# Kernel optimization log

Measured on AMD Instinct MI355X. Metric: run time of the kernel, lower is better.

Reference implementation:

```python
import jax, jax.numpy as jnp
import numpy as np

N, E, F_IN, HID, L, G = 50000, 800000, 128, 64, 3, 512
BN_EPS = 1e-5


def setup_inputs() -> dict:
    key = jax.random.key(0)
    ks = jax.random.split(key, 8)
    x = jax.random.normal(ks[0], (N, F_IN), dtype=jnp.float32)
    edge_index = jax.random.randint(ks[1], (2, E), 0, N, dtype=jnp.int32)
    batch = jnp.sort(jax.random.randint(ks[2], (N,), 0, G, dtype=jnp.int32))
    # params (Glorot-ish init for weights; BN init per module: gamma=1, beta=1e-4)
    W_feat = jax.random.normal(ks[3], (F_IN, HID), dtype=jnp.float32) / np.sqrt(F_IN)
    b_feat = jnp.zeros((HID,), jnp.float32)
    Ws = jax.random.normal(ks[4], (L, HID, HID), dtype=jnp.float32) / np.sqrt(HID)
    bs = jnp.zeros((L, HID), jnp.float32)
    bn_feat_g = jnp.ones((F_IN,), jnp.float32)
    bn_feat_b = jnp.full((F_IN,), 1e-4, jnp.float32)
    bn_g = jnp.ones((L, HID), jnp.float32)
    bn_b = jnp.full((L, HID), 1e-4, jnp.float32)
    return {"x": x, "edge_index": edge_index, "batch": batch,
            "bn_feat_g": bn_feat_g, "bn_feat_b": bn_feat_b,
            "W_feat": W_feat, "b_feat": b_feat,
            "bn_g": bn_g, "bn_b": bn_b, "Ws": Ws, "bs": bs}


def batch_norm(x, gamma, beta):
    # training-mode BatchNorm1d: biased variance over the node dimension
    mu = jnp.mean(x, axis=0)
    var = jnp.mean(jnp.square(x - mu), axis=0)
    return (x - mu) * jax.lax.rsqrt(var + BN_EPS) * gamma + beta


def gcn_conv(h, W, b, src, dst):
    # h: [N, d_in] -> linear then normalized gather-scatter with self-loops
    h = h @ W  # [N, d_out]
    n = h.shape[0]
    loop = jnp.arange(n, dtype=src.dtype)
    row = jnp.concatenate([src, loop])  # source (j)
    col = jnp.concatenate([dst, loop])  # target (i)
    w = jnp.ones(row.shape[0], h.dtype)
    deg = jax.ops.segment_sum(w, row, num_segments=n)  # PyG: deg over row
    dis = jnp.where(deg > 0, jax.lax.rsqrt(jnp.maximum(deg, 1.0)), 0.0)
    norm = dis[row] * w * dis[col]  # [E+N]
    out = jax.ops.segment_sum(norm[:, None] * h[row], col, num_segments=n)
    return out + b


def reference(x, edge_index, batch, bn_feat_g, bn_feat_b, W_feat, b_feat,
              bn_g, bn_b, Ws, bs):
    src, dst = edge_index[0], edge_index[1]
    h = batch_norm(x, bn_feat_g, bn_feat_b)
    h = jax.nn.relu(h @ W_feat + b_feat)  # conv_feat has gfn=True -> plain linear
    for i in range(L):
        h = batch_norm(h, bn_g[i], bn_b[i])
        h = jax.nn.relu(gcn_conv(h, Ws[i], bs[i], src, dst))
    graph_emb = jax.ops.segment_sum(h, batch, num_segments=G)  # global_add_pool
    return graph_emb
```

## Files before the change

### kernel.cpp

```cpp
#include <hip/hip_runtime.h>
#include <math.h>

#define HID 64
#define BN_EPS 1e-5f
#define NBMAX 256

typedef unsigned int uint;
typedef unsigned short ushort;


__global__ __launch_bounds__(256) void k_bucket_hist(const int* __restrict__ ei, int E, int NB,
                                                     int* __restrict__ bcnt_d, int* __restrict__ bcnt_s) {
    __shared__ int hd[NBMAX], hs[NBMAX];
    int t = threadIdx.x;
    if (t < NB) { hd[t] = 0; hs[t] = 0; }
    __syncthreads();
    for (int e = blockIdx.x * 256 + t; e < E; e += gridDim.x * 256) {
        int src = ei[e], dst = ei[E + e];
        atomicAdd(&hs[src >> 8], 1);
        atomicAdd(&hd[dst >> 8], 1);
    }
    __syncthreads();
    if (t < NB) {
        if (hd[t]) atomicAdd(&bcnt_d[t], hd[t]);
        if (hs[t]) atomicAdd(&bcnt_s[t], hs[t]);
    }
}

__global__ __launch_bounds__(256) void k_bucket_scan(const int* __restrict__ bcnt_d, const int* __restrict__ bcnt_s,
                                                     int NB, int N, int E,
                                                     int* __restrict__ bbase_d, int* __restrict__ cursor_d,
                                                     int* __restrict__ bbase_s, int* __restrict__ cursor_s,
                                                     int* __restrict__ rowptr) {
    __shared__ int sh[256];
    int t = threadIdx.x;
    int v = (t < NB) ? bcnt_d[t] : 0;
    sh[t] = v; __syncthreads();
    for (int s = 1; s < 256; s <<= 1) { int u = (t >= s) ? sh[t - s] : 0; __syncthreads(); sh[t] += u; __syncthreads(); }
    int excl = sh[t] - v;
    if (t <= NB) bbase_d[t] = excl;
    if (t < NB) cursor_d[t] = excl;
    if (t == 0) rowptr[N] = E;
    __syncthreads();
    v = (t < NB) ? bcnt_s[t] : 0;
    sh[t] = v; __syncthreads();
    for (int s = 1; s < 256; s <<= 1) { int u = (t >= s) ? sh[t - s] : 0; __syncthreads(); sh[t] += u; __syncthreads(); }
    excl = sh[t] - v;
    if (t <= NB) bbase_s[t] = excl;
    if (t < NB) cursor_s[t] = excl;
}

__global__ __launch_bounds__(256) void k_scatter_stats(const int* __restrict__ ei, int E, int NB, int SCB,
                                                       int* __restrict__ cursor_d, int* __restrict__ cursor_s,
                                                       uint* __restrict__ bedge, int* __restrict__ bsrc,
                                                       const float* __restrict__ X, int n,
                                                       float* __restrict__ spartial) {
    __shared__ __align__(16) char smemraw[8192];
    int t = threadIdx.x;
    if ((int)blockIdx.x < SCB) {
        int* hd = (int*)smemraw;
        int* hs = hd + 256;
        int* curd = hs + 256;
        int* curs = curd + 256;
        int chunk = (E + SCB - 1) / SCB;
        int e0 = blockIdx.x * chunk;
        int e1 = min(e0 + chunk, E);
        if (t < NB) { hd[t] = 0; hs[t] = 0; }
        __syncthreads();
        for (int e = e0 + t; e < e1; e += 256) {
            int src = ei[e], dst = ei[E + e];
            atomicAdd(&hd[dst >> 8], 1);
            atomicAdd(&hs[src >> 8], 1);
        }
        __syncthreads();
        if (t < NB) {
            curd[t] = hd[t] ? atomicAdd(&cursor_d[t], hd[t]) : 0;
            curs[t] = hs[t] ? atomicAdd(&cursor_s[t], hs[t]) : 0;
        }
        __syncthreads();
        for (int e = e0 + t; e < e1; e += 256) {
            int src = ei[e], dst = ei[E + e];
            int pd = atomicAdd(&curd[dst >> 8], 1);
            bedge[pd] = ((uint)(dst & 255) << 16) | (uint)src;
            int ps = atomicAdd(&curs[src >> 8], 1);
            bsrc[ps] = src;
        }
    } else {
        int b = blockIdx.x - SCB;
        int SB = gridDim.x - SCB;
        float4* shs = (float4*)smemraw;
        float4* shq = shs + 256;
        int c4 = t & 31, rsub = t >> 5;
        float4 s = make_float4(0.f, 0.f, 0.f, 0.f);
        float4 q = make_float4(0.f, 0.f, 0.f, 0.f);
        for (int r = b * 8 + rsub; r < n; r += SB * 8) {
            float4 v = ((const float4*)X)[(size_t)r * 32 + c4];
            s.x += v.x; s.y += v.y; s.z += v.z; s.w += v.w;
            q.x = fmaf(v.x, v.x, q.x); q.y = fmaf(v.y, v.y, q.y);
            q.z = fmaf(v.z, v.z, q.z); q.w = fmaf(v.w, v.w, q.w);
        }
        shs[t] = s; shq[t] = q;
        __syncthreads();
        if (rsub == 0) {
            #pragma unroll
            for (int k = 1; k < 8; k++) {
                float4 a = shs[t + k * 32], bq = shq[t + k * 32];
                s.x += a.x; s.y += a.y; s.z += a.z; s.w += a.w;
                q.x += bq.x; q.y += bq.y; q.z += bq.z; q.w += bq.w;
            }
            float* p = spartial + (size_t)b * 256;
            ((float4*)p)[c4] = s;
            ((float4*)(p + 128))[c4] = q;
        }
    }
}

__global__ __launch_bounds__(256) void k_build_csr_outdeg_statsf(
        const uint* __restrict__ bedge, const int* __restrict__ bbase_d,
        const int* __restrict__ bsrc, const int* __restrict__ bbase_s,
        int N, int NB,
        int* __restrict__ rowptr, int* __restrict__ eidx, float* __restrict__ dis,
        const float* __restrict__ spartial, int snblocks, float* __restrict__ stats) {
    __shared__ int h[256], off[256], cur[256];
    int t = threadIdx.x, b = blockIdx.x;
    if (b < NB) {
        int base = bbase_d[b], end = bbase_d[b + 1];
        h[t] = 0; __syncthreads();
        for (int p = base + t; p < end; p += 256)
            atomicAdd(&h[(int)(bedge[p] >> 16) & 255], 1);
        __syncthreads();
        off[t] = h[t]; __syncthreads();
        for (int s = 1; s < 256; s <<= 1) { int u = (t >= s) ? off[t - s] : 0; __syncthreads(); off[t] += u; __syncthreads(); }
        int excl = off[t] - h[t];
        int node = (b << 8) + t;
        if (node <= N) rowptr[node] = base + excl;
        cur[t] = excl; __syncthreads();
        for (int p = base + t; p < end; p += 256) {
            uint be = bedge[p];
            int bin = (int)(be >> 16) & 255;
            int pos = atomicAdd(&cur[bin], 1);
            eidx[base + pos] = (int)(be & 0xffffu);
        }
    } else if (b < 2 * NB) {
        int b2 = b - NB;
        int base = bbase_s[b2], end = bbase_s[b2 + 1];
        h[t] = 0; __syncthreads();
        for (int p = base + t; p < end; p += 256) atomicAdd(&h[bsrc[p] & 255], 1);
        __syncthreads();
        int node = (b2 << 8) + t;
        if (node < N) dis[node] = rsqrtf((float)(h[t] + 1));
    } else {
        int j = b - 2 * NB;
        float* sh = (float*)h;
        float acc = 0.f;
        for (int bb = t; bb < snblocks; bb += 256) acc += spartial[(size_t)bb * 256 + j];
        sh[t] = acc;
        __syncthreads();
        #pragma unroll
        for (int o = 128; o > 0; o >>= 1) {
            if (t < o) sh[t] += sh[t + o];
            __syncthreads();
        }
        if (t == 0) stats[j] = sh[0];
    }
}

template <int F>
__global__ __launch_bounds__(256) void k_stats_final(const float* __restrict__ partial, int nblocks,
                                                     float* __restrict__ stats) {
    int j = blockIdx.x;
    int t = threadIdx.x;
    float acc = 0.f;
    for (int b = t; b < nblocks; b += 256) acc += partial[(size_t)b * (2 * F) + j];
    __shared__ float sh[256];
    sh[t] = acc;
    __syncthreads();
    #pragma unroll
    for (int off = 128; off > 0; off >>= 1) {
        if (t < off) sh[t] += sh[t + off];
        __syncthreads();
    }
    if (t == 0) stats[j] = sh[0];
}


__device__ inline uint bf16pk(float a, float b) {
    uint ua = __builtin_bit_cast(uint, a);
    ua += 0x7fff + ((ua >> 16) & 1);
    uint ub = __builtin_bit_cast(uint, b);
    ub += 0x7fff + ((ub >> 16) & 1);
    return (ua >> 16) | (ub & 0xffff0000u);
}
__device__ inline float bfl(uint v) { return __builtin_bit_cast(float, v << 16); }
__device__ inline float bfh(uint v) { return __builtin_bit_cast(float, v & 0xffff0000u); }

template <int K, bool RELU, bool DIS, bool STATS, bool HASB>
__global__ __launch_bounds__(256) void k_gemm(const float* __restrict__ X, const float* __restrict__ W,
                                              const float* __restrict__ stats,
                                              const float* __restrict__ gamma, const float* __restrict__ beta,
                                              const float* __restrict__ bias0, const float* __restrict__ dis,
                                              float n_inv, void* __restrict__ out, int n,
                                              float* __restrict__ spartial) {
    constexpr int KC = 64;
    constexpr int XS = 68;
    __shared__ float Xs[KC * XS];
    __shared__ float Wsm[KC * HID];
    __shared__ float As[128], Cs[128];

    int t = threadIdx.x;
    int tx = t & 15, ty = t >> 4;
    int row0 = blockIdx.x * 64;

    if (t < K) {
        float mu = stats[t] * n_inv;
        float var = stats[K + t] * n_inv - mu * mu;
        float a = gamma[t] * rsqrtf(var + BN_EPS);
        As[t] = a;
        Cs[t] = beta[t] - mu * a;
    }
    __syncthreads();

    float acc[4][4];
    #pragma unroll
    for (int i = 0; i < 4; i++)
        #pragma unroll
        for (int j = 0; j < 4; j++) acc[i][j] = 0.f;
    float4 bp = make_float4(0.f, 0.f, 0.f, 0.f);

    for (int kc = 0; kc < K; kc += KC) {
        #pragma unroll
        for (int it = 0; it < 4; ++it) {
            int id = t + 256 * it;
            int r = id >> 4, c4 = id & 15;
            float4 v = make_float4(0.f, 0.f, 0.f, 0.f);
            if (row0 + r < n) v = *(const float4*)(X + (size_t)(row0 + r) * K + kc + 4 * c4);
            int kk = 4 * c4;
            Xs[(kk + 0) * XS + r] = v.x;
            Xs[(kk + 1) * XS + r] = v.y;
            Xs[(kk + 2) * XS + r] = v.z;
            Xs[(kk + 3) * XS + r] = v.w;
        }
        {
            const float4* wsrc = (const float4*)(W + (size_t)kc * HID);
            #pragma unroll
            for (int it = 0; it < 4; ++it) {
                int id = t + 256 * it;
                int kl = id >> 4;
                float4 raw = wsrc[id];
                float a = As[kc + kl], c = Cs[kc + kl];
                float4 sc;
                sc.x = a * raw.x; sc.y = a * raw.y; sc.z = a * raw.z; sc.w = a * raw.w;
                ((float4*)Wsm)[id] = sc;
                bp.x = fmaf(c, raw.x, bp.x);
                bp.y = fmaf(c, raw.y, bp.y);
                bp.z = fmaf(c, raw.z, bp.z);
                bp.w = fmaf(c, raw.w, bp.w);
            }
        }
        __syncthreads();
        #pragma unroll 8
        for (int k = 0; k < KC; ++k) {
            float4 xv = *(const float4*)&Xs[k * XS + 4 * ty];
            float4 wv = *(const float4*)&Wsm[k * HID + 4 * tx];
            acc[0][0] = fmaf(xv.x, wv.x, acc[0][0]);
            acc[0][1] = fmaf(xv.x, wv.y, acc[0][1]);
            acc[0][2] = fmaf(xv.x, wv.z, acc[0][2]);
            acc[0][3] = fmaf(xv.x, wv.w, acc[0][3]);
            acc[1][0] = fmaf(xv.y, wv.x, acc[1][0]);
            acc[1][1] = fmaf(xv.y, wv.y, acc[1][1]);
            acc[1][2] = fmaf(xv.y, wv.z, acc[1][2]);
            acc[1][3] = fmaf(xv.y, wv.w, acc[1][3]);
            acc[2][0] = fmaf(xv.z, wv.x, acc[2][0]);
            acc[2][1] = fmaf(xv.z, wv.y, acc[2][1]);
            acc[2][2] = fmaf(xv.z, wv.z, acc[2][2]);
            acc[2][3] = fmaf(xv.z, wv.w, acc[2][3]);
            acc[3][0] = fmaf(xv.w, wv.x, acc[3][0]);
            acc[3][1] = fmaf(xv.w, wv.y, acc[3][1]);
            acc[3][2] = fmaf(xv.w, wv.z, acc[3][2]);
            acc[3][3] = fmaf(xv.w, wv.w, acc[3][3]);
        }
        __syncthreads();
    }

    {
        float* redb = Xs + 2048;
        *(float4*)&redb[ty * 64 + 4 * tx] = bp;
        __syncthreads();
        if (t < 64) {
            float s = 0.f;
            #pragma unroll
            for (int k = 0; k < 16; ++k) s += redb[k * 64 + t];
            Xs[3072 + t] = s + (HASB ? bias0[t] : 0.f);
        }
        __syncthreads();
    }
    float4 bv = *(const float4*)&Xs[3072 + 4 * tx];

    float4 cs = make_float4(0.f, 0.f, 0.f, 0.f);
    float4 cq = make_float4(0.f, 0.f, 0.f, 0.f);
    #pragma unroll
    for (int i = 0; i < 4; ++i) {
        int row = row0 + 4 * ty + i;
        bool valid = row < n;
        float vx = acc[i][0] + bv.x, vy = acc[i][1] + bv.y;
        float vz = acc[i][2] + bv.z, vw = acc[i][3] + bv.w;
        if constexpr (DIS) {
            if (valid) {
                float d = dis[row];
                uint2 pk;
                pk.x = bf16pk(vx * d, vy * d);
                pk.y = bf16pk(vz * d, vw * d);
                *(uint2*)((ushort*)out + (size_t)row * HID + 4 * tx) = pk;
            }
        } else {
            float4 v;
            v.x = RELU ? fmaxf(vx, 0.f) : vx;
            v.y = RELU ? fmaxf(vy, 0.f) : vy;
            v.z = RELU ? fmaxf(vz, 0.f) : vz;
            v.w = RELU ? fmaxf(vw, 0.f) : vw;
            if (valid) {
                *(float4*)((float*)out + (size_t)row * HID + 4 * tx) = v;
                if constexpr (STATS) {
                    cs.x += v.x; cs.y += v.y; cs.z += v.z; cs.w += v.w;
                    cq.x = fmaf(v.x, v.x, cq.x); cq.y = fmaf(v.y, v.y, cq.y);
                    cq.z = fmaf(v.z, v.z, cq.z); cq.w = fmaf(v.w, v.w, cq.w);
                }
            }
        }
    }
    if constexpr (STATS) {
        __syncthreads();
        float* reds = Xs;
        float* redq = Xs + 1024;
        *(float4*)&reds[ty * 64 + 4 * tx] = cs;
        *(float4*)&redq[ty * 64 + 4 * tx] = cq;
        __syncthreads();
        if (t < 64) {
            float s = 0.f, q = 0.f;
            #pragma unroll
            for (int k = 0; k < 16; ++k) { s += reds[k * 64 + t]; q += redq[k * 64 + t]; }
            spartial[(size_t)blockIdx.x * 128 + t] = s;
            spartial[(size_t)blockIdx.x * 128 + 64 + t] = q;
        }
    }
}


template <bool STATS>
__global__ __launch_bounds__(256) void k_agg(const ushort* __restrict__ s, const int* __restrict__ rowptr,
                                             const int* __restrict__ eidx, const float* __restrict__ dis,
                                             const float* __restrict__ bias, float* __restrict__ out, int n,
                                             float* __restrict__ spartial) {
    int t = threadIdx.x;
    int nl = t >> 5;
    int li = t & 31;
    int i = blockIdx.x * 8 + nl;
    int f = li * 2;
    float2 r = make_float2(0.f, 0.f);
    bool valid = i < n;
    if (valid) {
        const uint* sp = (const uint*)s;
        uint v = sp[(size_t)i * 32 + li];
        float ax = bfl(v), ay = bfh(v);
        int q = rowptr[i], qe = rowptr[i + 1];
        for (; q + 8 <= qe; q += 8) {
            int j0 = eidx[q], j1 = eidx[q + 1], j2 = eidx[q + 2], j3 = eidx[q + 3];
            int j4 = eidx[q + 4], j5 = eidx[q + 5], j6 = eidx[q + 6], j7 = eidx[q + 7];
            uint v0 = sp[(size_t)j0 * 32 + li];
            uint v1 = sp[(size_t)j1 * 32 + li];
            uint v2 = sp[(size_t)j2 * 32 + li];
            uint v3 = sp[(size_t)j3 * 32 + li];
            uint v4 = sp[(size_t)j4 * 32 + li];
            uint v5 = sp[(size_t)j5 * 32 + li];
            uint v6 = sp[(size_t)j6 * 32 + li];
            uint v7 = sp[(size_t)j7 * 32 + li];
            ax += ((bfl(v0) + bfl(v1)) + (bfl(v2) + bfl(v3))) + ((bfl(v4) + bfl(v5)) + (bfl(v6) + bfl(v7)));
            ay += ((bfh(v0) + bfh(v1)) + (bfh(v2) + bfh(v3))) + ((bfh(v4) + bfh(v5)) + (bfh(v6) + bfh(v7)));
        }
        for (; q + 4 <= qe; q += 4) {
            int j0 = eidx[q], j1 = eidx[q + 1], j2 = eidx[q + 2], j3 = eidx[q + 3];
            uint v0 = sp[(size_t)j0 * 32 + li];
            uint v1 = sp[(size_t)j1 * 32 + li];
            uint v2 = sp[(size_t)j2 * 32 + li];
            uint v3 = sp[(size_t)j3 * 32 + li];
            ax += (bfl(v0) + bfl(v1)) + (bfl(v2) + bfl(v3));
            ay += (bfh(v0) + bfh(v1)) + (bfh(v2) + bfh(v3));
        }
        for (; q < qe; ++q) {
            uint vv = sp[(size_t)eidx[q] * 32 + li];
            ax += bfl(vv); ay += bfh(vv);
        }
        float dd = dis[i];
        float2 bb = *(const float2*)(bias + f);
        r.x = fmaxf(fmaf(dd, ax, bb.x), 0.f);
        r.y = fmaxf(fmaf(dd, ay, bb.y), 0.f);
        *(float2*)(out + (size_t)i * HID + f) = r;
    }
    if constexpr (STATS) {
        __shared__ float sh[8 * 64 * 2];
        sh[nl * 64 + f] = r.x;
        sh[nl * 64 + f + 1] = r.y;
        sh[512 + nl * 64 + f] = r.x * r.x;
        sh[512 + nl * 64 + f + 1] = r.y * r.y;
        __syncthreads();
        if (t < 64) {
            float ss = 0.f, qq = 0.f;
            #pragma unroll
            for (int k = 0; k < 8; ++k) { ss += sh[k * 64 + t]; qq += sh[512 + k * 64 + t]; }
            spartial[(size_t)blockIdx.x * 128 + t] = ss;
            spartial[(size_t)blockIdx.x * 128 + 64 + t] = qq;
        }
    }
}


__global__ __launch_bounds__(256) void k_pool(const float* __restrict__ h, const int* __restrict__ batch,
                                              int n, float* __restrict__ out) {
    int g = blockIdx.x;
    int lo = 0, hi = n;
    while (lo < hi) { int mid = (lo + hi) >> 1; if (batch[mid] < g) lo = mid + 1; else hi = mid; }
    int start = lo;
    hi = n;
    while (lo < hi) { int mid = (lo + hi) >> 1; if (batch[mid] < g + 1) lo = mid + 1; else hi = mid; }
    int end = lo;
    int lane = threadIdx.x & 63;
    int rs = threadIdx.x >> 6;
    float acc = 0.f;
    for (int r = start + rs; r < end; r += 4) acc += h[(size_t)r * HID + lane];
    __shared__ float sh[256];
    sh[threadIdx.x] = acc;
    __syncthreads();
    if (threadIdx.x < 64) {
        acc = sh[threadIdx.x] + sh[64 + threadIdx.x] + sh[128 + threadIdx.x] + sh[192 + threadIdx.x];
        out[(size_t)g * HID + threadIdx.x] = acc;
    }
}


extern "C" void kernel_launch(void* const* d_in, const int* in_sizes, int n_in,
                              void* d_out, int out_size, void* d_ws, size_t ws_size,
                              hipStream_t stream) {
    const float* x     = (const float*)d_in[0];
    const int*   ei    = (const int*)d_in[1];
    const int*   batch = (const int*)d_in[2];
    const float* bnfg  = (const float*)d_in[3];
    const float* bnfb  = (const float*)d_in[4];
    const float* Wfeat = (const float*)d_in[5];
    const float* bfeat = (const float*)d_in[6];
    const float* bng   = (const float*)d_in[7];
    const float* bnb   = (const float*)d_in[8];
    const float* Ws    = (const float*)d_in[9];
    const float* bs    = (const float*)d_in[10];
    float* out = (float*)d_out;

    const int N   = in_sizes[2];
    const int E   = in_sizes[1] / 2;
    const int L   = in_sizes[9] / (HID * HID);
    const int G   = out_size / HID;
    const int NB  = (N + 255) >> 8;
    const int SCB = 256;
    const int SB  = 512;
    const int gG  = (N + 63) / 64;
    const int gA  = (N + 7) / 8;
    const float n_inv = 1.f / (float)N;

    char* w = (char*)d_ws;
    auto alloc = [&](size_t bytes) { char* p = w; w += (bytes + 255) & ~(size_t)255; return p; };
    int*   bcnt_d = (int*)alloc(256 * 4);
    int*   bcnt_s = (int*)alloc(256 * 4);
    size_t zero_bytes = (size_t)(w - (char*)d_ws);
    float* stats    = (float*)alloc(1024 * 4);
    size_t spmax    = (size_t)(SB > gA ? SB : gA) * 256 * 4;
    float* spartial = (float*)alloc(spmax);
    int*   bbase_d  = (int*)alloc(257 * 4);
    int*   cursor_d = (int*)alloc(256 * 4);
    int*   bbase_s  = (int*)alloc(257 * 4);
    int*   cursor_s = (int*)alloc(256 * 4);
    int*   rowptr   = (int*)alloc(((size_t)N + 1) * 4);
    int*   eidx     = (int*)alloc((size_t)E * 4);
    float* dis      = (float*)alloc((size_t)N * 4);
    float* bufA     = (float*)alloc((size_t)N * HID * 4);
    ushort* bufB    = (ushort*)alloc((size_t)N * HID * 2);
    uint* bedge = (uint*)bufA;
    int*  bsrc  = (int*)bufB;

    hipMemsetAsync(d_ws, 0, zero_bytes, stream);

    k_bucket_hist<<<512, 256, 0, stream>>>(ei, E, NB, bcnt_d, bcnt_s);
    k_bucket_scan<<<1, 256, 0, stream>>>(bcnt_d, bcnt_s, NB, N, E,
                                         bbase_d, cursor_d, bbase_s, cursor_s, rowptr);
    k_scatter_stats<<<SCB + SB, 256, 0, stream>>>(ei, E, NB, SCB, cursor_d, cursor_s,
                                                  bedge, bsrc, x, N, spartial);
    k_build_csr_outdeg_statsf<<<2 * NB + 256, 256, 0, stream>>>(
        bedge, bbase_d, bsrc, bbase_s, N, NB, rowptr, eidx, dis, spartial, SB, stats);

    k_gemm<128, true, false, true, true><<<gG, 256, 0, stream>>>(
        x, Wfeat, stats, bnfg, bnfb, bfeat, nullptr, n_inv, (void*)bufA, N, spartial);
    int spblocks = gG;

    for (int l = 0; l < L; ++l) {
        k_stats_final<64><<<128, 256, 0, stream>>>(spartial, spblocks, stats);
        k_gemm<64, false, true, false, false><<<gG, 256, 0, stream>>>(
            bufA, Ws + (size_t)l * HID * HID, stats, bng + (size_t)l * HID, bnb + (size_t)l * HID,
            nullptr, dis, n_inv, (void*)bufB, N, nullptr);
        if (l < L - 1) {
            k_agg<true><<<gA, 256, 0, stream>>>(bufB, rowptr, eidx, dis, bs + (size_t)l * HID, bufA, N, spartial);
            spblocks = gA;
        } else {
            k_agg<false><<<gA, 256, 0, stream>>>(bufB, rowptr, eidx, dis, bs + (size_t)l * HID, bufA, N, nullptr);
        }
    }

    k_pool<<<G, 256, 0, stream>>>(bufA, batch, N, out);
}
```

Measured before the change: 298.7 us.

## Fuse stats reductions via atomics, merge hist+scan, fuse pooling into last aggregation

Merges the bucket histogram and scan into one kernel using a last-block-done counter. Replaces per-block partial buffers plus separate final-reduction kernels with float atomicAdds straight into the stats arrays, which removes the k_stats_final launches. The final aggregation now accumulates global_add_pool directly through atomics over runs of sorted batch ids, so the k_pool kernel and the last feature write go away. The aggregation kernel is also restructured so each node is handled by 4 edge slots × 8 lanes using uint4 loads, with shuffle reductions. The trade-offs are atomic contention and nondeterministic float summation order.

```diff
diff --git a/kernel.cpp b/kernel.cpp
--- a/kernel.cpp
+++ b/kernel.cpp
@@ -9,11 +9,27 @@
 typedef unsigned short ushort;
 
 
-__global__ __launch_bounds__(256) void k_bucket_hist(const int* __restrict__ ei, int E, int NB,
-                                                     int* __restrict__ bcnt_d, int* __restrict__ bcnt_s) {
-    __shared__ int hd[NBMAX], hs[NBMAX];
+__device__ inline uint bf16pk(float a, float b) {
+    uint ua = __builtin_bit_cast(uint, a);
+    ua += 0x7fff + ((ua >> 16) & 1);
+    uint ub = __builtin_bit_cast(uint, b);
+    ub += 0x7fff + ((ub >> 16) & 1);
+    return (ua >> 16) | (ub & 0xffff0000u);
+}
+__device__ inline float bfl(uint v) { return __builtin_bit_cast(float, v << 16); }
+__device__ inline float bfh(uint v) { return __builtin_bit_cast(float, v & 0xffff0000u); }
+
+
+__global__ __launch_bounds__(256) void k_hist_scan(const int* __restrict__ ei, int E, int NB, int N,
+                                                   int* __restrict__ bcnt_d, int* __restrict__ bcnt_s,
+                                                   int* __restrict__ done,
+                                                   int* __restrict__ bbase_d, int* __restrict__ cursor_d,
+                                                   int* __restrict__ bbase_s, int* __restrict__ cursor_s,
+                                                   int* __restrict__ rowptr) {
+    __shared__ int hd[256], hs[256];
+    __shared__ int lastFlag;
     int t = threadIdx.x;
-    if (t < NB) { hd[t] = 0; hs[t] = 0; }
+    hd[t] = 0; hs[t] = 0;
     __syncthreads();
     for (int e = blockIdx.x * 256 + t; e < E; e += gridDim.x * 256) {
         int src = ei[e], dst = ei[E + e];
@@ -25,27 +41,23 @@
         if (hd[t]) atomicAdd(&bcnt_d[t], hd[t]);
         if (hs[t]) atomicAdd(&bcnt_s[t], hs[t]);
     }
-}
-
-__global__ __launch_bounds__(256) void k_bucket_scan(const int* __restrict__ bcnt_d, const int* __restrict__ bcnt_s,
-                                                     int NB, int N, int E,
-                                                     int* __restrict__ bbase_d, int* __restrict__ cursor_d,
-                                                     int* __restrict__ bbase_s, int* __restrict__ cursor_s,
-                                                     int* __restrict__ rowptr) {
-    __shared__ int sh[256];
-    int t = threadIdx.x;
-    int v = (t < NB) ? bcnt_d[t] : 0;
-    sh[t] = v; __syncthreads();
-    for (int s = 1; s < 256; s <<= 1) { int u = (t >= s) ? sh[t - s] : 0; __syncthreads(); sh[t] += u; __syncthreads(); }
-    int excl = sh[t] - v;
+    __threadfence();
+    __syncthreads();
+    if (t == 0) lastFlag = (atomicAdd(done, 1) == (int)gridDim.x - 1);
+    __syncthreads();
+    if (!lastFlag) return;
+    int v = (t < NB) ? atomicAdd(&bcnt_d[t], 0) : 0;
+    hd[t] = v; __syncthreads();
+    for (int s = 1; s < 256; s <<= 1) { int u = (t >= s) ? hd[t - s] : 0; __syncthreads(); hd[t] += u; __syncthreads(); }
+    int excl = hd[t] - v;
     if (t <= NB) bbase_d[t] = excl;
     if (t < NB) cursor_d[t] = excl;
     if (t == 0) rowptr[N] = E;
     __syncthreads();
-    v = (t < NB) ? bcnt_s[t] : 0;
-    sh[t] = v; __syncthreads();
-    for (int s = 1; s < 256; s <<= 1) { int u = (t >= s) ? sh[t - s] : 0; __syncthreads(); sh[t] += u; __syncthreads(); }
-    excl = sh[t] - v;
+    v = (t < NB) ? atomicAdd(&bcnt_s[t], 0) : 0;
+    hs[t] = v; __syncthreads();
+    for (int s = 1; s < 256; s <<= 1) { int u = (t >= s) ? hs[t - s] : 0; __syncthreads(); hs[t] += u; __syncthreads(); }
+    excl = hs[t] - v;
     if (t <= NB) bbase_s[t] = excl;
     if (t < NB) cursor_s[t] = excl;
 }
@@ -54,7 +66,7 @@
                                                        int* __restrict__ cursor_d, int* __restrict__ cursor_s,
                                                        uint* __restrict__ bedge, int* __restrict__ bsrc,
                                                        const float* __restrict__ X, int n,
-                                                       float* __restrict__ spartial) {
+                                                       float* __restrict__ stats) {
     __shared__ __align__(16) char smemraw[8192];
     int t = threadIdx.x;
     if ((int)blockIdx.x < SCB) {
@@ -108,19 +120,19 @@
                 s.x += a.x; s.y += a.y; s.z += a.z; s.w += a.w;
                 q.x += bq.x; q.y += bq.y; q.z += bq.z; q.w += bq.w;
             }
-            float* p = spartial + (size_t)b * 256;
-            ((float4*)p)[c4] = s;
-            ((float4*)(p + 128))[c4] = q;
-        }
-    }
-}
-
-__global__ __launch_bounds__(256) void k_build_csr_outdeg_statsf(
+            atomicAdd(&stats[4 * t + 0], s.x); atomicAdd(&stats[4 * t + 1], s.y);
+            atomicAdd(&stats[4 * t + 2], s.z); atomicAdd(&stats[4 * t + 3], s.w);
+            atomicAdd(&stats[128 + 4 * t + 0], q.x); atomicAdd(&stats[128 + 4 * t + 1], q.y);
+            atomicAdd(&stats[128 + 4 * t + 2], q.z); atomicAdd(&stats[128 + 4 * t + 3], q.w);
+        }
+    }
+}
+
+__global__ __launch_bounds__(256) void k_build_csr_outdeg(
         const uint* __restrict__ bedge, const int* __restrict__ bbase_d,
         const int* __restrict__ bsrc, const int* __restrict__ bbase_s,
         int N, int NB,
-        int* __restrict__ rowptr, int* __restrict__ eidx, float* __restrict__ dis,
-        const float* __restrict__ spartial, int snblocks, float* __restrict__ stats) {
+        int* __restrict__ rowptr, int* __restrict__ eidx, float* __restrict__ dis) {
     __shared__ int h[256], off[256], cur[256];
     int t = threadIdx.x, b = blockIdx.x;
     if (b < NB) {
@@ -141,7 +153,7 @@
             int pos = atomicAdd(&cur[bin], 1);
             eidx[base + pos] = (int)(be & 0xffffu);
         }
-    } else if (b < 2 * NB) {
+    } else {
         int b2 = b - NB;
         int base = bbase_s[b2], end = bbase_s[b2 + 1];
         h[t] = 0; __syncthreads();
@@ -149,50 +161,9 @@
         __syncthreads();
         int node = (b2 << 8) + t;
         if (node < N) dis[node] = rsqrtf((float)(h[t] + 1));
-    } else {
-        int j = b - 2 * NB;
-        float* sh = (float*)h;
-        float acc = 0.f;
-        for (int bb = t; bb < snblocks; bb += 256) acc += spartial[(size_t)bb * 256 + j];
-        sh[t] = acc;
-        __syncthreads();
-        #pragma unroll
-        for (int o = 128; o > 0; o >>= 1) {
-            if (t < o) sh[t] += sh[t + o];
-            __syncthreads();
-        }
-        if (t == 0) stats[j] = sh[0];
-    }
-}
-
-template <int F>
-__global__ __launch_bounds__(256) void k_stats_final(const float* __restrict__ partial, int nblocks,
-                                                     float* __restrict__ stats) {
-    int j = blockIdx.x;
-    int t = threadIdx.x;
-    float acc = 0.f;
-    for (int b = t; b < nblocks; b += 256) acc += partial[(size_t)b * (2 * F) + j];
-    __shared__ float sh[256];
-    sh[t] = acc;
-    __syncthreads();
-    #pragma unroll
-    for (int off = 128; off > 0; off >>= 1) {
-        if (t < off) sh[t] += sh[t + off];
-        __syncthreads();
-    }
-    if (t == 0) stats[j] = sh[0];
-}
-
-
-__device__ inline uint bf16pk(float a, float b) {
-    uint ua = __builtin_bit_cast(uint, a);
-    ua += 0x7fff + ((ua >> 16) & 1);
-    uint ub = __builtin_bit_cast(uint, b);
-    ub += 0x7fff + ((ub >> 16) & 1);
-    return (ua >> 16) | (ub & 0xffff0000u);
-}
-__device__ inline float bfl(uint v) { return __builtin_bit_cast(float, v << 16); }
-__device__ inline float bfh(uint v) { return __builtin_bit_cast(float, v & 0xffff0000u); }
+    }
+}
+
 
 template <int K, bool RELU, bool DIS, bool STATS, bool HASB>
 __global__ __launch_bounds__(256) void k_gemm(const float* __restrict__ X, const float* __restrict__ W,
@@ -200,7 +171,7 @@
                                               const float* __restrict__ gamma, const float* __restrict__ beta,
                                               const float* __restrict__ bias0, const float* __restrict__ dis,
                                               float n_inv, void* __restrict__ out, int n,
-                                              float* __restrict__ spartial) {
+                                              float* __restrict__ sout) {
     constexpr int KC = 64;
     constexpr int XS = 68;
     __shared__ float Xs[KC * XS];
@@ -339,100 +310,121 @@
             float s = 0.f, q = 0.f;
             #pragma unroll
             for (int k = 0; k < 16; ++k) { s += reds[k * 64 + t]; q += redq[k * 64 + t]; }
-            spartial[(size_t)blockIdx.x * 128 + t] = s;
-            spartial[(size_t)blockIdx.x * 128 + 64 + t] = q;
-        }
-    }
-}
-
-
-template <bool STATS>
+            atomicAdd(&sout[t], s);
+            atomicAdd(&sout[64 + t], q);
+        }
+    }
+}
+
+
+template <bool POOL>
 __global__ __launch_bounds__(256) void k_agg(const ushort* __restrict__ s, const int* __restrict__ rowptr,
                                              const int* __restrict__ eidx, const float* __restrict__ dis,
                                              const float* __restrict__ bias, float* __restrict__ out, int n,
-                                             float* __restrict__ spartial) {
+                                             float* __restrict__ sout, const int* __restrict__ batch,
+                                             float* __restrict__ pool_out) {
+    __shared__ float shs[8 * 64];
+    __shared__ float shq[8 * 64];
+    __shared__ int ib[8];
     int t = threadIdx.x;
     int nl = t >> 5;
     int li = t & 31;
+    int slot = li >> 3;
+    int c = li & 7;
     int i = blockIdx.x * 8 + nl;
-    int f = li * 2;
-    float2 r = make_float2(0.f, 0.f);
+    const uint4* sp4 = (const uint4*)s;
+    float a[8];
+    #pragma unroll
+    for (int k = 0; k < 8; ++k) a[k] = 0.f;
     bool valid = i < n;
     if (valid) {
-        const uint* sp = (const uint*)s;
-        uint v = sp[(size_t)i * 32 + li];
-        float ax = bfl(v), ay = bfh(v);
-        int q = rowptr[i], qe = rowptr[i + 1];
-        for (; q + 8 <= qe; q += 8) {
-            int j0 = eidx[q], j1 = eidx[q + 1], j2 = eidx[q + 2], j3 = eidx[q + 3];
-            int j4 = eidx[q + 4], j5 = eidx[q + 5], j6 = eidx[q + 6], j7 = eidx[q + 7];
-            uint v0 = sp[(size_t)j0 * 32 + li];
-            uint v1 = sp[(size_t)j1 * 32 + li];
-            uint v2 = sp[(size_t)j2 * 32 + li];
-            uint v3 = sp[(size_t)j3 * 32 + li];
-            uint v4 = sp[(size_t)j4 * 32 + li];
-            uint v5 = sp[(size_t)j5 * 32 + li];
-            uint v6 = sp[(size_t)j6 * 32 + li];
-            uint v7 = sp[(size_t)j7 * 32 + li];
-            ax += ((bfl(v0) + bfl(v1)) + (bfl(v2) + bfl(v3))) + ((bfl(v4) + bfl(v5)) + (bfl(v6) + bfl(v7)));
-            ay += ((bfh(v0) + bfh(v1)) + (bfh(v2) + bfh(v3))) + ((bfh(v4) + bfh(v5)) + (bfh(v6) + bfh(v7)));
-        }
-        for (; q + 4 <= qe; q += 4) {
-            int j0 = eidx[q], j1 = eidx[q + 1], j2 = eidx[q + 2], j3 = eidx[q + 3];
-            uint v0 = sp[(size_t)j0 * 32 + li];
-            uint v1 = sp[(size_t)j1 * 32 + li];
-            uint v2 = sp[(size_t)j2 * 32 + li];
-            uint v3 = sp[(size_t)j3 * 32 + li];
-            ax += (bfl(v0) + bfl(v1)) + (bfl(v2) + bfl(v3));
-            ay += (bfh(v0) + bfh(v1)) + (bfh(v2) + bfh(v3));
-        }
-        for (; q < qe; ++q) {
-            uint vv = sp[(size_t)eidx[q] * 32 + li];
-            ax += bfl(vv); ay += bfh(vv);
-        }
-        float dd = dis[i];
-        float2 bb = *(const float2*)(bias + f);
-        r.x = fmaxf(fmaf(dd, ax, bb.x), 0.f);
-        r.y = fmaxf(fmaf(dd, ay, bb.y), 0.f);
-        *(float2*)(out + (size_t)i * HID + f) = r;
-    }
-    if constexpr (STATS) {
-        __shared__ float sh[8 * 64 * 2];
-        sh[nl * 64 + f] = r.x;
-        sh[nl * 64 + f + 1] = r.y;
-        sh[512 + nl * 64 + f] = r.x * r.x;
-        sh[512 + nl * 64 + f + 1] = r.y * r.y;
-        __syncthreads();
-        if (t < 64) {
+        int q = rowptr[i] + slot;
+        int qe = rowptr[i + 1];
+        while (q + 4 < qe) {
+            int j0 = eidx[q], j1 = eidx[q + 4];
+            uint4 v0 = sp4[(size_t)j0 * 8 + c];
+            uint4 v1 = sp4[(size_t)j1 * 8 + c];
+            q += 8;
+            a[0] += bfl(v0.x) + bfl(v1.x); a[1] += bfh(v0.x) + bfh(v1.x);
+            a[2] += bfl(v0.y) + bfl(v1.y); a[3] += bfh(v0.y) + bfh(v1.y);
+            a[4] += bfl(v0.z) + bfl(v1.z); a[5] += bfh(v0.z) + bfh(v1.z);
+            a[6] += bfl(v0.w) + bfl(v1.w); a[7] += bfh(v0.w) + bfh(v1.w);
+        }
+        if (q < qe) {
+            int j0 = eidx[q];
+            uint4 v0 = sp4[(size_t)j0 * 8 + c];
+            a[0] += bfl(v0.x); a[1] += bfh(v0.x);
+            a[2] += bfl(v0.y); a[3] += bfh(v0.y);
+            a[4] += bfl(v0.z); a[5] += bfh(v0.z);
+            a[6] += bfl(v0.w); a[7] += bfh(v0.w);
+        }
+    }
+    #pragma unroll
+    for (int k = 0; k < 8; ++k) a[k] += __shfl_xor(a[k], 8);
+    #pragma unroll
+    for (int k = 0; k < 8; ++k) a[k] += __shfl_xor(a[k], 16);
+
+    if (li < 8) {
+        float r[8];
+        if (valid) {
+            uint4 v = sp4[(size_t)i * 8 + c];
+            a[0] += bfl(v.x); a[1] += bfh(v.x);
+            a[2] += bfl(v.y); a[3] += bfh(v.y);
+            a[4] += bfl(v.z); a[5] += bfh(v.z);
+            a[6] += bfl(v.w); a[7] += bfh(v.w);
+            float d = dis[i];
+            float4 b0 = *(const float4*)(bias + 8 * c);
+            float4 b1 = *(const float4*)(bias + 8 * c + 4);
+            r[0] = fmaxf(fmaf(d, a[0], b0.x), 0.f);
+            r[1] = fmaxf(fmaf(d, a[1], b0.y), 0.f);
+            r[2] = fmaxf(fmaf(d, a[2], b0.z), 0.f);
+            r[3] = fmaxf(fmaf(d, a[3], b0.w), 0.f);
+            r[4] = fmaxf(fmaf(d, a[4], b1.x), 0.f);
+            r[5] = fmaxf(fmaf(d, a[5], b1.y), 0.f);
+            r[6] = fmaxf(fmaf(d, a[6], b1.z), 0.f);
+            r[7] = fmaxf(fmaf(d, a[7], b1.w), 0.f);
+            if constexpr (!POOL) {
+                *(float4*)(out + (size_t)i * HID + 8 * c)     = make_float4(r[0], r[1], r[2], r[3]);
+                *(float4*)(out + (size_t)i * HID + 8 * c + 4) = make_float4(r[4], r[5], r[6], r[7]);
+            }
+        } else {
+            #pragma unroll
+            for (int k = 0; k < 8; ++k) r[k] = 0.f;
+        }
+        #pragma unroll
+        for (int k = 0; k < 8; ++k) shs[nl * 64 + 8 * c + k] = r[k];
+        if constexpr (!POOL) {
+            #pragma unroll
+            for (int k = 0; k < 8; ++k) shq[nl * 64 + 8 * c + k] = r[k] * r[k];
+        }
+    }
+    if constexpr (POOL) {
+        if (li == 0) ib[nl] = valid ? batch[i] : -1;
+    }
+    __syncthreads();
+    if (t < 64) {
+        if constexpr (!POOL) {
             float ss = 0.f, qq = 0.f;
             #pragma unroll
-            for (int k = 0; k < 8; ++k) { ss += sh[k * 64 + t]; qq += sh[512 + k * 64 + t]; }
-            spartial[(size_t)blockIdx.x * 128 + t] = ss;
-            spartial[(size_t)blockIdx.x * 128 + 64 + t] = qq;
-        }
-    }
-}
-
-
-__global__ __launch_bounds__(256) void k_pool(const float* __restrict__ h, const int* __restrict__ batch,
-                                              int n, float* __restrict__ out) {
-    int g = blockIdx.x;
-    int lo = 0, hi = n;
-    while (lo < hi) { int mid = (lo + hi) >> 1; if (batch[mid] < g) lo = mid + 1; else hi = mid; }
-    int start = lo;
-    hi = n;
-    while (lo < hi) { int mid = (lo + hi) >> 1; if (batch[mid] < g + 1) lo = mid + 1; else hi = mid; }
-    int end = lo;
-    int lane = threadIdx.x & 63;
-    int rs = threadIdx.x >> 6;
-    float acc = 0.f;
-    for (int r = start + rs; r < end; r += 4) acc += h[(size_t)r * HID + lane];
-    __shared__ float sh[256];
-    sh[threadIdx.x] = acc;
-    __syncthreads();
-    if (threadIdx.x < 64) {
-        acc = sh[threadIdx.x] + sh[64 + threadIdx.x] + sh[128 + threadIdx.x] + sh[192 + threadIdx.x];
-        out[(size_t)g * HID + threadIdx.x] = acc;
+            for (int k = 0; k < 8; ++k) { ss += shs[k * 64 + t]; qq += shq[k * 64 + t]; }
+            atomicAdd(&sout[t], ss);
+            atomicAdd(&sout[64 + t], qq);
+        } else {
+            int g = ib[0];
+            float run = shs[t];
+            #pragma unroll
+            for (int k = 1; k < 8; ++k) {
+                int gk = ib[k];
+                float v = shs[k * 64 + t];
+                if (gk == g) {
+                    run += v;
+                } else {
+                    if (g >= 0) atomicAdd(&pool_out[(size_t)g * HID + t], run);
+                    g = gk; run = v;
+                }
+            }
+            if (g >= 0) atomicAdd(&pool_out[(size_t)g * HID + t], run);
+        }
     }
 }
 
@@ -456,7 +448,6 @@
     const int N   = in_sizes[2];
     const int E   = in_sizes[1] / 2;
     const int L   = in_sizes[9] / (HID * HID);
-    const int G   = out_size / HID;
     const int NB  = (N + 255) >> 8;
     const int SCB = 256;
     const int SB  = 512;
@@ -468,10 +459,9 @@
     auto alloc = [&](size_t bytes) { char* p = w; w += (bytes + 255) & ~(size_t)255; return p; };
     int*   bcnt_d = (int*)alloc(256 * 4);
     int*   bcnt_s = (int*)alloc(256 * 4);
+    int*   done   = (int*)alloc(256);
+    float* stats  = (float*)alloc(1024 * 4);
     size_t zero_bytes = (size_t)(w - (char*)d_ws);
-    float* stats    = (float*)alloc(1024 * 4);
-    size_t spmax    = (size_t)(SB > gA ? SB : gA) * 256 * 4;
-    float* spartial = (float*)alloc(spmax);
     int*   bbase_d  = (int*)alloc(257 * 4);
     int*   cursor_d = (int*)alloc(256 * 4);
     int*   bbase_s  = (int*)alloc(257 * 4);
@@ -485,31 +475,29 @@
     int*  bsrc  = (int*)bufB;
 
     hipMemsetAsync(d_ws, 0, zero_bytes, stream);
-
-    k_bucket_hist<<<512, 256, 0, stream>>>(ei, E, NB, bcnt_d, bcnt_s);
-    k_bucket_scan<<<1, 256, 0, stream>>>(bcnt_d, bcnt_s, NB, N, E,
+    hipMemsetAsync(d_out, 0, (size_t)out_size * sizeof(float), stream);
+
+    k_hist_scan<<<512, 256, 0, stream>>>(ei, E, NB, N, bcnt_d, bcnt_s, done,
                                          bbase_d, cursor_d, bbase_s, cursor_s, rowptr);
     k_scatter_stats<<<SCB + SB, 256, 0, stream>>>(ei, E, NB, SCB, cursor_d, cursor_s,
-                                                  bedge, bsrc, x, N, spartial);
-    k_build_csr_outdeg_statsf<<<2 * NB + 256, 256, 0, stream>>>(
-        bedge, bbase_d, bsrc, bbase_s, N, NB, rowptr, eidx, dis, spartial, SB, stats);
+                                                  bedge, bsrc, x, N, stats);
+    k_build_csr_outdeg<<<2 * NB, 256, 0, stream>>>(bedge, bbase_d, bsrc, bbase_s, N, NB,
+                                                   rowptr, eidx, dis);
 
     k_gemm<128, true, false, true, true><<<gG, 256, 0, stream>>>(
-        x, Wfeat, stats, bnfg, bnfb, bfeat, nullptr, n_inv, (void*)bufA, N, spartial);
-    int spblocks = gG;
+        x, Wfeat, stats, bnfg, bnfb, bfeat, nullptr, n_inv, (void*)bufA, N, stats + 256);
 
     for (int l = 0; l < L; ++l) {
-        k_stats_final<64><<<128, 256, 0, stream>>>(spartial, spblocks, stats);
         k_gemm<64, false, true, false, false><<<gG, 256, 0, stream>>>(
-            bufA, Ws + (size_t)l * HID * HID, stats, bng + (size_t)l * HID, bnb + (size_t)l * HID,
+            bufA, Ws + (size_t)l * HID * HID, stats + 256 + 128 * l,
+            bng + (size_t)l * HID, bnb + (size_t)l * HID,
             nullptr, dis, n_inv, (void*)bufB, N, nullptr);
         if (l < L - 1) {
-            k_agg<true><<<gA, 256, 0, stream>>>(bufB, rowptr, eidx, dis, bs + (size_t)l * HID, bufA, N, spartial);
-            spblocks = gA;
+            k_agg<false><<<gA, 256, 0, stream>>>(bufB, rowptr, eidx, dis, bs + (size_t)l * HID,
+                                                 bufA, N, stats + 256 + 128 * (l + 1), nullptr, nullptr);
         } else {
-            k_agg<false><<<gA, 256, 0, stream>>>(bufB, rowptr, eidx, dis, bs + (size_t)l * HID, bufA, N, nullptr);
-        }
-    }
-
-    k_pool<<<G, 256, 0, stream>>>(bufA, batch, N, out);
-}
+            k_agg<true><<<gA, 256, 0, stream>>>(bufB, rowptr, eidx, dis, bs + (size_t)l * HID,
+                                                nullptr, N, nullptr, batch, out);
+        }
+    }
+}
```

After: 615.3 us. 106% more time.
